# Kernel tuning notes

Measured on AMD Instinct MI355X. Metric: run time of the kernel, lower is better.

## Reference

```python
import jax, jax.numpy as jnp
import numpy as np

N_NODES = 100000
N_EDGES = 3200000
IN_CH, HID, OUT_CH = 128, 16, 64


def gcn_conv(x, W, b, row, col, n_nodes):
    # PyG GCNConv: add self loops, symmetric deg^{-1/2} normalization,
    # linear transform, scatter-add aggregation at target nodes (col).
    x = x @ W  # [N, out]
    deg = jax.ops.segment_sum(jnp.ones_like(col, dtype=x.dtype), col,
                              num_segments=n_nodes)  # includes self loops
    inv_sqrt = jnp.where(deg > 0, jax.lax.rsqrt(deg), 0.0)
    norm = inv_sqrt[row] * inv_sqrt[col]  # [E+N]
    msgs = x[row] * norm[:, None]  # gather + scale
    out = jax.ops.segment_sum(msgs, col, num_segments=n_nodes)
    return out + b


def setup_inputs() -> dict:
    key = jax.random.key(0)
    ks = jax.random.split(key, 12)
    x = jax.random.normal(ks[0], (N_NODES, IN_CH), dtype=jnp.float32)
    edge_index = jax.random.randint(ks[1], (2, N_EDGES), 0, N_NODES, dtype=jnp.int64)

    def glorot(k, fan_in, fan_out):
        s = jnp.sqrt(6.0 / (fan_in + fan_out))
        return jax.random.uniform(k, (fan_in, fan_out), jnp.float32, -s, s)

    return {
        'x': x,
        'edge_index': edge_index,
        'conv1_W': glorot(ks[2], IN_CH, HID),
        'conv1_b': jnp.zeros((HID,), jnp.float32),
        'conv2_W': glorot(ks[3], HID, OUT_CH),
        'conv2_b': jnp.zeros((OUT_CH,), jnp.float32),
        't1_W': glorot(ks[4], IN_CH, HID),
        't1_b': jnp.zeros((HID,), jnp.float32),
        't2_W': glorot(ks[5], HID, OUT_CH),
        't2_b': jnp.zeros((OUT_CH,), jnp.float32),
    }


def reference(x, edge_index, conv1_W, conv1_b, conv2_W, conv2_b,
              t1_W, t1_b, t2_W, t2_b):
    n = x.shape[0]
    # add self loops once (fixed shape)
    loops = jnp.arange(n, dtype=edge_index.dtype)
    row = jnp.concatenate([edge_index[0], loops])
    col = jnp.concatenate([edge_index[1], loops])

    identity1 = x @ t1_W + t1_b
    h = jax.nn.relu(gcn_conv(x, conv1_W, conv1_b, row, col, n)) + identity1
    identity2 = h @ t2_W + t2_b
    out = jax.nn.relu(gcn_conv(h, conv2_W, conv2_b, row, col, n)) + identity2
    return out
```

## Files before the change

kernel.cpp:

```cpp
#include <hip/hip_runtime.h>

#define INCH 128
#define C1   16
#define C2   64
#define LOCB 7
#define BNODES (1 << LOCB)
#define CAP  8192
#define ROWBITS 17
#define ROWMASK ((1 << ROWBITS) - 1)
#define SENT 0xFFFFFFFFu

typedef int iv4 __attribute__((ext_vector_type(4)));

__device__ __forceinline__ unsigned short f2bf(float f) {
    unsigned u = __float_as_uint(f);
    return (unsigned short)((u + 0x7FFF + ((u >> 16) & 1)) >> 16);
}
__device__ __forceinline__ float bf2f(unsigned short s) {
    return __uint_as_float((unsigned)s << 16);
}

__global__ void binit_kernel(int* __restrict__ gcur, int K) {
    int t = blockIdx.x * blockDim.x + threadIdx.x;
    if (t < K) gcur[t] = t * CAP;
}

__global__ __launch_bounds__(256) void bucket_kernel(
    const int* __restrict__ row, const int* __restrict__ col,
    int* __restrict__ gcur, int* __restrict__ barr,
    int e, int n, int K, int nblocks)
{
    __shared__ int cnt[1024];
    __shared__ int cur[1024];
    __shared__ int sst[1024];
    int e4 = e >> 2;
    long b0 = (long)blockIdx.x * e4 / nblocks;
    long b1 = (long)(blockIdx.x + 1) * e4 / nblocks;
    const iv4* c4p = (const iv4*)col;
    const iv4* r4p = (const iv4*)row;
    for (int i = threadIdx.x; i < 1024; i += 256) cnt[i] = 0;
    __syncthreads();
    for (long i = b0 + threadIdx.x; i < b1; i += 256) {
        iv4 c4 = c4p[i], r4 = r4p[i];
        #pragma unroll
        for (int k = 0; k < 4; ++k) {
            unsigned c = (unsigned)c4[k], r = (unsigned)r4[k];
            if (c < (unsigned)n && r < (unsigned)n)
                atomicAdd(&cnt[c >> LOCB], 1);
        }
    }
    if (blockIdx.x == 0) {
        for (int i = e4 * 4 + threadIdx.x; i < e; i += 256) {
            unsigned c = (unsigned)col[i], r = (unsigned)row[i];
            if (c < (unsigned)n && r < (unsigned)n)
                atomicAdd(&cnt[c >> LOCB], 1);
        }
    }
    __syncthreads();
    for (int i = threadIdx.x; i < K; i += 256) {
        int c = cnt[i];
        int start = c ? atomicAdd(&gcur[i], (c + 15) & ~15) : 0;
        cur[i] = start;
        sst[i] = start;
    }
    __syncthreads();
    for (long i = b0 + threadIdx.x; i < b1; i += 256) {
        iv4 c4 = c4p[i], r4 = r4p[i];
        #pragma unroll
        for (int k = 0; k < 4; ++k) {
            unsigned c = (unsigned)c4[k], r = (unsigned)r4[k];
            if (c < (unsigned)n && r < (unsigned)n) {
                int b = c >> LOCB;
                int slot = atomicAdd(&cur[b], 1);
                if ((unsigned)slot < (unsigned)((b + 1) * CAP))
                    barr[slot] = (int)(r | ((c & (BNODES - 1)) << ROWBITS));
            }
        }
    }
    if (blockIdx.x == 0) {
        for (int i = e4 * 4 + threadIdx.x; i < e; i += 256) {
            unsigned c = (unsigned)col[i], r = (unsigned)row[i];
            if (c < (unsigned)n && r < (unsigned)n) {
                int b = c >> LOCB;
                int slot = atomicAdd(&cur[b], 1);
                if ((unsigned)slot < (unsigned)((b + 1) * CAP))
                    barr[slot] = (int)(r | ((c & (BNODES - 1)) << ROWBITS));
            }
        }
    }
    __syncthreads();
    for (int i = threadIdx.x; i < K; i += 256) {
        int c = cnt[i];
        if (!c) continue;
        int start = sst[i];
        int end = start + c;
        int re  = start + ((c + 15) & ~15);
        int lim = (i + 1) * CAP;
        if (end > lim) end = lim;
        if (re  > lim) re  = lim;
        for (int j = end; j < re; ++j) barr[j] = (int)SENT;
    }
}

__global__ __launch_bounds__(1024) void bucket_scan_kernel(
    const int* __restrict__ gcur, int* __restrict__ bbase, int K)
{
    __shared__ int tmp[1024];
    int t = threadIdx.x;
    int len = 0;
    if (t < K) {
        int l = gcur[t] - t * CAP;
        len = (l < 0) ? 0 : (l > CAP ? CAP : l);
    }
    tmp[t] = len;
    __syncthreads();
    for (int off = 1; off < 1024; off <<= 1) {
        int v = (t >= off) ? tmp[t - off] : 0;
        __syncthreads();
        tmp[t] += v;
        __syncthreads();
    }
    if (t < K) bbase[t] = tmp[t] - len;
}

__global__ __launch_bounds__(256) void sort_kernel(
    const int* __restrict__ barr, const int* __restrict__ gcur,
    const int* __restrict__ bbase,
    int* __restrict__ cnt, int* __restrict__ offs, float* __restrict__ inv,
    int* __restrict__ sorted, int n)
{
    __shared__ int lcnt[BNODES];
    __shared__ int lcur[BNODES];
    __shared__ int tmp[BNODES];
    int b = blockIdx.x;
    int tid = threadIdx.x;
    if (tid < BNODES) lcnt[tid] = 0;
    __syncthreads();
    int base = b * CAP;
    int len = gcur[b] - base;
    if (len < 0) len = 0;
    if (len > CAP) len = CAP;
    int len4 = len >> 2;
    const iv4* b4 = (const iv4*)(barr + base);
    for (int i = tid; i < len4; i += 256) {
        iv4 p4 = b4[i];
        #pragma unroll
        for (int k = 0; k < 4; ++k) {
            unsigned pk = (unsigned)p4[k];
            if ((pk & ROWMASK) < (unsigned)n)
                atomicAdd(&lcnt[(pk >> ROWBITS) & (BNODES - 1)], 1);
        }
    }
    for (int i = len4 * 4 + tid; i < len; i += 256) {
        unsigned pk = (unsigned)barr[base + i];
        if ((pk & ROWMASK) < (unsigned)n)
            atomicAdd(&lcnt[(pk >> ROWBITS) & (BNODES - 1)], 1);
    }
    __syncthreads();
    int v = (tid < BNODES) ? lcnt[tid] : 0;
    if (tid < BNODES) tmp[tid] = v;
    __syncthreads();
    for (int off = 1; off < BNODES; off <<= 1) {
        int t2 = (tid < BNODES && tid >= off) ? tmp[tid - off] : 0;
        __syncthreads();
        if (tid < BNODES) tmp[tid] += t2;
        __syncthreads();
    }
    int gbase = bbase[b];
    if (tid < BNODES) {
        int exc = tmp[tid] - v;
        lcur[tid] = exc;
        int node = (b << LOCB) + tid;
        if (node < n) {
            cnt[node]  = v;
            offs[node] = gbase + exc;
            inv[node]  = rsqrtf((float)(v + 1));
        }
    }
    __syncthreads();
    for (int i = tid; i < len4; i += 256) {
        iv4 p4 = b4[i];
        #pragma unroll
        for (int k = 0; k < 4; ++k) {
            unsigned pk = (unsigned)p4[k];
            if ((pk & ROWMASK) < (unsigned)n) {
                int loc = (pk >> ROWBITS) & (BNODES - 1);
                int pos = atomicAdd(&lcur[loc], 1);
                if ((unsigned)pos < (unsigned)CAP)
                    sorted[gbase + pos] = (int)(pk & ROWMASK);
            }
        }
    }
    for (int i = len4 * 4 + tid; i < len; i += 256) {
        unsigned pk = (unsigned)barr[base + i];
        if ((pk & ROWMASK) < (unsigned)n) {
            int loc = (pk >> ROWBITS) & (BNODES - 1);
            int pos = atomicAdd(&lcur[loc], 1);
            if ((unsigned)pos < (unsigned)CAP)
                sorted[gbase + pos] = (int)(pk & ROWMASK);
        }
    }
}

__global__ __launch_bounds__(256) void linear1_kernel(
    const float* __restrict__ x, const float* __restrict__ W1,
    const float* __restrict__ T1, const float* __restrict__ t1b,
    const float* __restrict__ inv,
    unsigned short* __restrict__ xW1s_bf, float* __restrict__ xT1, int n)
{
    __shared__ float Wc[INCH][32];
    __shared__ float xs[16][INCH + 4];
    int tid = threadIdx.x;

    for (int i = tid; i < INCH * C1; i += 256) {
        int k = i / C1, c = i % C1;
        Wc[k][c]      = W1[i];
        Wc[k][c + 16] = T1[i];
    }
    int node0 = blockIdx.x * 16;
    for (int i = tid; i < 16 * (INCH / 4); i += 256) {
        int r = i / (INCH / 4);
        int cc = i % (INCH / 4);
        int node = node0 + r;
        float4 v = make_float4(0.f, 0.f, 0.f, 0.f);
        if (node < n) v = ((const float4*)x)[(size_t)node * (INCH / 4) + cc];
        ((float4*)&xs[r][0])[cc] = v;
    }
    __syncthreads();

    int ch = tid & 15, nl = tid >> 4;
    int node = node0 + nl;
    if (node >= n) return;
    float a1 = 0.f, a2 = 0.f;
    #pragma unroll
    for (int k = 0; k < INCH; ++k) {
        float xv = xs[nl][k];
        a1 += xv * Wc[k][ch];
        a2 += xv * Wc[k][ch + 16];
    }
    xW1s_bf[(node << 4) + ch] = f2bf(a1 * inv[node]);
    xT1[(node << 4) + ch]     = a2 + t1b[ch];
}

__global__ __launch_bounds__(256) void agg1_csr_kernel(
    const int* __restrict__ sorted, const int* __restrict__ offs,
    const int* __restrict__ cnt, const float* __restrict__ inv,
    const unsigned short* __restrict__ xW1s_bf, const float* __restrict__ xT1,
    const float* __restrict__ b1,
    float* __restrict__ h, unsigned short* __restrict__ hs_bf, int n)
{
    int node = blockIdx.x * 16 + (threadIdx.x >> 4);
    int ch = threadIdx.x & 15;
    if (node >= n) return;
    int beg = offs[node], end = beg + cnt[node];
    float ic = inv[node];
    float a0 = 0.f, a1 = 0.f, a2 = 0.f, a3 = 0.f;
    int p = beg;
    for (; p + 7 < end; p += 8) {
        int s0 = sorted[p],     s1 = sorted[p + 1];
        int s2 = sorted[p + 2], s3 = sorted[p + 3];
        int s4 = sorted[p + 4], s5 = sorted[p + 5];
        int s6 = sorted[p + 6], s7 = sorted[p + 7];
        a0 += bf2f(xW1s_bf[(s0 << 4) + ch]);
        a1 += bf2f(xW1s_bf[(s1 << 4) + ch]);
        a2 += bf2f(xW1s_bf[(s2 << 4) + ch]);
        a3 += bf2f(xW1s_bf[(s3 << 4) + ch]);
        a0 += bf2f(xW1s_bf[(s4 << 4) + ch]);
        a1 += bf2f(xW1s_bf[(s5 << 4) + ch]);
        a2 += bf2f(xW1s_bf[(s6 << 4) + ch]);
        a3 += bf2f(xW1s_bf[(s7 << 4) + ch]);
    }
    for (; p < end; ++p) a0 += bf2f(xW1s_bf[(sorted[p] << 4) + ch]);
    int idx = (node << 4) + ch;
    float v = (a0 + a1 + a2 + a3 + bf2f(xW1s_bf[idx])) * ic + b1[ch];
    float hv = fmaxf(v, 0.f) + xT1[idx];
    h[idx]     = hv;
    hs_bf[idx] = f2bf(hv * ic);
}

__global__ __launch_bounds__(256) void agg2_fused_kernel(
    const int* __restrict__ sorted, const int* __restrict__ offs,
    const int* __restrict__ cnt, const float* __restrict__ inv,
    const unsigned short* __restrict__ hs_bf, const float* __restrict__ h,
    const float* __restrict__ W2, const float* __restrict__ T2,
    const float* __restrict__ b2, const float* __restrict__ t2b,
    float* __restrict__ out, int n)
{
    __shared__ float Wc[C1][128];
    __shared__ float acc_s[16][C1];
    __shared__ float h_s[16][C1];
    int tid = threadIdx.x;

    for (int i = tid; i < C1 * 128; i += 256) {
        int k = i >> 7, c = i & 127;
        Wc[k][c] = (c < 64) ? W2[k * C2 + c] : T2[k * C2 + (c - 64)];
    }

    int nl = tid >> 4, ch = tid & 15;
    int node = blockIdx.x * 16 + nl;
    float acc = 0.f, hval = 0.f;
    if (node < n) {
        int beg = offs[node], end = beg + cnt[node];
        float a0 = 0.f, a1 = 0.f, a2 = 0.f, a3 = 0.f;
        int p = beg;
        for (; p + 7 < end; p += 8) {
            int s0 = sorted[p],     s1 = sorted[p + 1];
            int s2 = sorted[p + 2], s3 = sorted[p + 3];
            int s4 = sorted[p + 4], s5 = sorted[p + 5];
            int s6 = sorted[p + 6], s7 = sorted[p + 7];
            a0 += bf2f(hs_bf[(s0 << 4) + ch]);
            a1 += bf2f(hs_bf[(s1 << 4) + ch]);
            a2 += bf2f(hs_bf[(s2 << 4) + ch]);
            a3 += bf2f(hs_bf[(s3 << 4) + ch]);
            a0 += bf2f(hs_bf[(s4 << 4) + ch]);
            a1 += bf2f(hs_bf[(s5 << 4) + ch]);
            a2 += bf2f(hs_bf[(s6 << 4) + ch]);
            a3 += bf2f(hs_bf[(s7 << 4) + ch]);
        }
        for (; p < end; ++p) a0 += bf2f(hs_bf[(sorted[p] << 4) + ch]);
        int idx = (node << 4) + ch;
        acc = (a0 + a1 + a2 + a3 + bf2f(hs_bf[idx])) * inv[node];
        hval = h[idx];
    }
    acc_s[nl][ch] = acc;
    h_s[nl][ch]   = hval;
    __syncthreads();

    int och = tid & 63, grp = tid >> 6;
    #pragma unroll
    for (int q = 0; q < 4; ++q) {
        int nl2 = grp * 4 + q;
        int node2 = blockIdx.x * 16 + nl2;
        if (node2 >= n) continue;
        float s1v = b2[och], s2v = t2b[och];
        #pragma unroll
        for (int k = 0; k < C1; ++k) {
            s1v += acc_s[nl2][k] * Wc[k][och];
            s2v += h_s[nl2][k]   * Wc[k][och + 64];
        }
        out[node2 * C2 + och] = fmaxf(s1v, 0.f) + s2v;
    }
}

extern "C" void kernel_launch(void* const* d_in, const int* in_sizes, int n_in,
                              void* d_out, int out_size, void* d_ws, size_t ws_size,
                              hipStream_t stream) {
    const float* x   = (const float*)d_in[0];
    const int*   ei  = (const int*)d_in[1];
    const float* W1  = (const float*)d_in[2];
    const float* b1  = (const float*)d_in[3];
    const float* W2  = (const float*)d_in[4];
    const float* b2  = (const float*)d_in[5];
    const float* T1  = (const float*)d_in[6];
    const float* t1b = (const float*)d_in[7];
    const float* T2  = (const float*)d_in[8];
    const float* t2b = (const float*)d_in[9];
    float* out = (float*)d_out;

    const int n = in_sizes[0] / INCH;
    const int e = in_sizes[1] / 2;
    const int* row = ei;
    const int* col = ei + e;
    const int K = (n + BNODES - 1) >> LOCB;

    char* ws = (char*)d_ws;
    int*   gcur  = (int*)ws;                          ws += 4096;
    int*   bbase = (int*)ws;                          ws += 4096;
    int*   cnt   = (int*)ws;                          ws += (size_t)n * 4;
    int*   offs  = (int*)ws;                          ws += (size_t)n * 4;
    float* inv   = (float*)ws;                        ws += (size_t)n * 4;
    float* xT1   = (float*)ws;                        ws += (size_t)n * C1 * 4;
    float* h     = (float*)ws;                        ws += (size_t)n * C1 * 4;
    unsigned short* xW1s_bf = (unsigned short*)ws;    ws += (size_t)n * C1 * 2;
    unsigned short* hs_bf   = (unsigned short*)ws;    ws += (size_t)n * C1 * 2;
    int*   sorted= (int*)ws;                          ws += (size_t)K * CAP * 4;
    int*   barr  = (int*)ws;                          ws += (size_t)K * CAP * 4;

    const int B = 256;
    const int nbb = 390;

    binit_kernel      <<<(K + B - 1) / B, B, 0, stream>>>(gcur, K);
    bucket_kernel     <<<nbb, B, 0, stream>>>(row, col, gcur, barr, e, n, K, nbb);
    bucket_scan_kernel<<<1, 1024, 0, stream>>>(gcur, bbase, K);
    sort_kernel       <<<K, B, 0, stream>>>(barr, gcur, bbase, cnt, offs, inv, sorted, n);

    linear1_kernel <<<(n + 15) / 16, B, 0, stream>>>(x, W1, T1, t1b, inv, xW1s_bf, xT1, n);
    agg1_csr_kernel<<<(n + 15) / 16, B, 0, stream>>>(sorted, offs, cnt, inv, xW1s_bf, xT1, b1, h, hs_bf, n);

    agg2_fused_kernel<<<(n + 15) / 16, B, 0, stream>>>(sorted, offs, cnt, inv, hs_bf, h,
                                                       W2, T2, b2, t2b, out, n);
}
```

Measured before the change: 303.5 us.

## Aggregate directly from destination buckets with LDS atomics, dropping CSR sort

```diff
diff --git a/kernel.cpp b/kernel.cpp
--- a/kernel.cpp
+++ b/kernel.cpp
@@ -9,8 +9,10 @@
 #define ROWBITS 17
 #define ROWMASK ((1 << ROWBITS) - 1)
 #define SENT 0xFFFFFFFFu
+#define ACCP 17
 
 typedef int iv4 __attribute__((ext_vector_type(4)));
+typedef unsigned short usv8 __attribute__((ext_vector_type(8)));
 
 __device__ __forceinline__ unsigned short f2bf(float f) {
     unsigned u = __float_as_uint(f);
@@ -102,38 +104,12 @@
     }
 }
 
-__global__ __launch_bounds__(1024) void bucket_scan_kernel(
-    const int* __restrict__ gcur, int* __restrict__ bbase, int K)
-{
-    __shared__ int tmp[1024];
-    int t = threadIdx.x;
-    int len = 0;
-    if (t < K) {
-        int l = gcur[t] - t * CAP;
-        len = (l < 0) ? 0 : (l > CAP ? CAP : l);
-    }
-    tmp[t] = len;
-    __syncthreads();
-    for (int off = 1; off < 1024; off <<= 1) {
-        int v = (t >= off) ? tmp[t - off] : 0;
-        __syncthreads();
-        tmp[t] += v;
-        __syncthreads();
-    }
-    if (t < K) bbase[t] = tmp[t] - len;
-}
-
-__global__ __launch_bounds__(256) void sort_kernel(
+__global__ __launch_bounds__(256) void degree_kernel(
     const int* __restrict__ barr, const int* __restrict__ gcur,
-    const int* __restrict__ bbase,
-    int* __restrict__ cnt, int* __restrict__ offs, float* __restrict__ inv,
-    int* __restrict__ sorted, int n)
+    float* __restrict__ inv, int n)
 {
     __shared__ int lcnt[BNODES];
-    __shared__ int lcur[BNODES];
-    __shared__ int tmp[BNODES];
-    int b = blockIdx.x;
-    int tid = threadIdx.x;
+    int b = blockIdx.x, tid = threadIdx.x;
     if (tid < BNODES) lcnt[tid] = 0;
     __syncthreads();
     int base = b * CAP;
@@ -157,48 +133,9 @@
             atomicAdd(&lcnt[(pk >> ROWBITS) & (BNODES - 1)], 1);
     }
     __syncthreads();
-    int v = (tid < BNODES) ? lcnt[tid] : 0;
-    if (tid < BNODES) tmp[tid] = v;
-    __syncthreads();
-    for (int off = 1; off < BNODES; off <<= 1) {
-        int t2 = (tid < BNODES && tid >= off) ? tmp[tid - off] : 0;
-        __syncthreads();
-        if (tid < BNODES) tmp[tid] += t2;
-        __syncthreads();
-    }
-    int gbase = bbase[b];
     if (tid < BNODES) {
-        int exc = tmp[tid] - v;
-        lcur[tid] = exc;
         int node = (b << LOCB) + tid;
-        if (node < n) {
-            cnt[node]  = v;
-            offs[node] = gbase + exc;
-            inv[node]  = rsqrtf((float)(v + 1));
-        }
-    }
-    __syncthreads();
-    for (int i = tid; i < len4; i += 256) {
-        iv4 p4 = b4[i];
-        #pragma unroll
-        for (int k = 0; k < 4; ++k) {
-            unsigned pk = (unsigned)p4[k];
-            if ((pk & ROWMASK) < (unsigned)n) {
-                int loc = (pk >> ROWBITS) & (BNODES - 1);
-                int pos = atomicAdd(&lcur[loc], 1);
-                if ((unsigned)pos < (unsigned)CAP)
-                    sorted[gbase + pos] = (int)(pk & ROWMASK);
-            }
-        }
-    }
-    for (int i = len4 * 4 + tid; i < len; i += 256) {
-        unsigned pk = (unsigned)barr[base + i];
-        if ((pk & ROWMASK) < (unsigned)n) {
-            int loc = (pk >> ROWBITS) & (BNODES - 1);
-            int pos = atomicAdd(&lcur[loc], 1);
-            if ((unsigned)pos < (unsigned)CAP)
-                sorted[gbase + pos] = (int)(pk & ROWMASK);
-        }
+        if (node < n) inv[node] = rsqrtf((float)lcnt[tid] + 1.0f);
     }
 }
 
@@ -242,103 +179,164 @@
     xT1[(node << 4) + ch]     = a2 + t1b[ch];
 }
 
-__global__ __launch_bounds__(256) void agg1_csr_kernel(
-    const int* __restrict__ sorted, const int* __restrict__ offs,
-    const int* __restrict__ cnt, const float* __restrict__ inv,
-    const unsigned short* __restrict__ xW1s_bf, const float* __restrict__ xT1,
-    const float* __restrict__ b1,
+#define SCATTER8(PK, SRC)                                                     \
+    do {                                                                      \
+        unsigned _s = (PK) & ROWMASK;                                         \
+        if (_s < un) {                                                        \
+            float* _a = &acc[((PK) >> ROWBITS) & (BNODES - 1)][chb];          \
+            _Pragma("unroll")                                                 \
+            for (int _j = 0; _j < 8; ++_j)                                    \
+                atomicAdd(&_a[_j], __uint_as_float((unsigned)(SRC)[_j] << 16)); \
+        }                                                                     \
+    } while (0)
+
+__global__ __launch_bounds__(256) void agg1_bucket_kernel(
+    const int* __restrict__ barr, const int* __restrict__ gcur,
+    const float* __restrict__ inv, const unsigned short* __restrict__ xW1s_bf,
+    const float* __restrict__ xT1, const float* __restrict__ b1,
     float* __restrict__ h, unsigned short* __restrict__ hs_bf, int n)
 {
-    int node = blockIdx.x * 16 + (threadIdx.x >> 4);
-    int ch = threadIdx.x & 15;
-    if (node >= n) return;
-    int beg = offs[node], end = beg + cnt[node];
-    float ic = inv[node];
-    float a0 = 0.f, a1 = 0.f, a2 = 0.f, a3 = 0.f;
-    int p = beg;
-    for (; p + 7 < end; p += 8) {
-        int s0 = sorted[p],     s1 = sorted[p + 1];
-        int s2 = sorted[p + 2], s3 = sorted[p + 3];
-        int s4 = sorted[p + 4], s5 = sorted[p + 5];
-        int s6 = sorted[p + 6], s7 = sorted[p + 7];
-        a0 += bf2f(xW1s_bf[(s0 << 4) + ch]);
-        a1 += bf2f(xW1s_bf[(s1 << 4) + ch]);
-        a2 += bf2f(xW1s_bf[(s2 << 4) + ch]);
-        a3 += bf2f(xW1s_bf[(s3 << 4) + ch]);
-        a0 += bf2f(xW1s_bf[(s4 << 4) + ch]);
-        a1 += bf2f(xW1s_bf[(s5 << 4) + ch]);
-        a2 += bf2f(xW1s_bf[(s6 << 4) + ch]);
-        a3 += bf2f(xW1s_bf[(s7 << 4) + ch]);
-    }
-    for (; p < end; ++p) a0 += bf2f(xW1s_bf[(sorted[p] << 4) + ch]);
-    int idx = (node << 4) + ch;
-    float v = (a0 + a1 + a2 + a3 + bf2f(xW1s_bf[idx])) * ic + b1[ch];
-    float hv = fmaxf(v, 0.f) + xT1[idx];
-    h[idx]     = hv;
-    hs_bf[idx] = f2bf(hv * ic);
-}
-
-__global__ __launch_bounds__(256) void agg2_fused_kernel(
-    const int* __restrict__ sorted, const int* __restrict__ offs,
-    const int* __restrict__ cnt, const float* __restrict__ inv,
-    const unsigned short* __restrict__ hs_bf, const float* __restrict__ h,
+    __shared__ float acc[BNODES][ACCP];
+    int b = blockIdx.x, tid = threadIdx.x;
+    for (int i = tid; i < BNODES * ACCP; i += 256) (&acc[0][0])[i] = 0.f;
+    __syncthreads();
+
+    int base = b * CAP;
+    int len = gcur[b] - base;
+    if (len < 0) len = 0;
+    if (len > CAP) len = CAP;
+    const int* bp = barr + base;
+    unsigned un = (unsigned)n;
+    int chb = (tid & 1) << 3;
+    int i = tid >> 1;
+    for (; i + 384 < len; i += 512) {
+        unsigned k0 = (unsigned)bp[i];
+        unsigned k1 = (unsigned)bp[i + 128];
+        unsigned k2 = (unsigned)bp[i + 256];
+        unsigned k3 = (unsigned)bp[i + 384];
+        unsigned s0 = k0 & ROWMASK, s1 = k1 & ROWMASK;
+        unsigned s2 = k2 & ROWMASK, s3 = k3 & ROWMASK;
+        unsigned c0 = s0 < un ? s0 : 0u, c1 = s1 < un ? s1 : 0u;
+        unsigned c2 = s2 < un ? s2 : 0u, c3 = s3 < un ? s3 : 0u;
+        usv8 v0 = *(const usv8*)(xW1s_bf + ((size_t)c0 << 4) + chb);
+        usv8 v1 = *(const usv8*)(xW1s_bf + ((size_t)c1 << 4) + chb);
+        usv8 v2 = *(const usv8*)(xW1s_bf + ((size_t)c2 << 4) + chb);
+        usv8 v3 = *(const usv8*)(xW1s_bf + ((size_t)c3 << 4) + chb);
+        SCATTER8(k0, v0);
+        SCATTER8(k1, v1);
+        SCATTER8(k2, v2);
+        SCATTER8(k3, v3);
+    }
+    for (; i < len; i += 128) {
+        unsigned k0 = (unsigned)bp[i];
+        unsigned s0 = k0 & ROWMASK;
+        if (s0 < un) {
+            usv8 v0 = *(const usv8*)(xW1s_bf + ((size_t)s0 << 4) + chb);
+            SCATTER8(k0, v0);
+        }
+    }
+    __syncthreads();
+
+    for (int t = tid; t < BNODES * C1; t += 256) {
+        int loc = t >> 4, ch = t & 15;
+        int node = (b << LOCB) + loc;
+        if (node >= n) continue;
+        int idx = (node << 4) + ch;
+        float ic = inv[node];
+        float v = (acc[loc][ch] + bf2f(xW1s_bf[idx])) * ic + b1[ch];
+        float hv = fmaxf(v, 0.f) + xT1[idx];
+        h[idx]     = hv;
+        hs_bf[idx] = f2bf(hv * ic);
+    }
+}
+
+__global__ __launch_bounds__(256) void agg2_bucket_kernel(
+    const int* __restrict__ barr, const int* __restrict__ gcur,
+    const float* __restrict__ inv, const unsigned short* __restrict__ hs_bf,
+    const float* __restrict__ h,
     const float* __restrict__ W2, const float* __restrict__ T2,
     const float* __restrict__ b2, const float* __restrict__ t2b,
     float* __restrict__ out, int n)
 {
+    __shared__ float acc[BNODES][ACCP];
     __shared__ float Wc[C1][128];
-    __shared__ float acc_s[16][C1];
-    __shared__ float h_s[16][C1];
-    int tid = threadIdx.x;
-
+    __shared__ float h_s[BNODES][C1];
+    int b = blockIdx.x, tid = threadIdx.x;
+    for (int i = tid; i < BNODES * ACCP; i += 256) (&acc[0][0])[i] = 0.f;
     for (int i = tid; i < C1 * 128; i += 256) {
         int k = i >> 7, c = i & 127;
         Wc[k][c] = (c < 64) ? W2[k * C2 + c] : T2[k * C2 + (c - 64)];
     }
-
-    int nl = tid >> 4, ch = tid & 15;
-    int node = blockIdx.x * 16 + nl;
-    float acc = 0.f, hval = 0.f;
-    if (node < n) {
-        int beg = offs[node], end = beg + cnt[node];
-        float a0 = 0.f, a1 = 0.f, a2 = 0.f, a3 = 0.f;
-        int p = beg;
-        for (; p + 7 < end; p += 8) {
-            int s0 = sorted[p],     s1 = sorted[p + 1];
-            int s2 = sorted[p + 2], s3 = sorted[p + 3];
-            int s4 = sorted[p + 4], s5 = sorted[p + 5];
-            int s6 = sorted[p + 6], s7 = sorted[p + 7];
-            a0 += bf2f(hs_bf[(s0 << 4) + ch]);
-            a1 += bf2f(hs_bf[(s1 << 4) + ch]);
-            a2 += bf2f(hs_bf[(s2 << 4) + ch]);
-            a3 += bf2f(hs_bf[(s3 << 4) + ch]);
-            a0 += bf2f(hs_bf[(s4 << 4) + ch]);
-            a1 += bf2f(hs_bf[(s5 << 4) + ch]);
-            a2 += bf2f(hs_bf[(s6 << 4) + ch]);
-            a3 += bf2f(hs_bf[(s7 << 4) + ch]);
-        }
-        for (; p < end; ++p) a0 += bf2f(hs_bf[(sorted[p] << 4) + ch]);
-        int idx = (node << 4) + ch;
-        acc = (a0 + a1 + a2 + a3 + bf2f(hs_bf[idx])) * inv[node];
-        hval = h[idx];
-    }
-    acc_s[nl][ch] = acc;
-    h_s[nl][ch]   = hval;
-    __syncthreads();
-
-    int och = tid & 63, grp = tid >> 6;
+    {
+        int node0 = b << LOCB;
+        for (int t = tid; t < BNODES * C1 / 4; t += 256) {
+            float4 v = make_float4(0.f, 0.f, 0.f, 0.f);
+            if (node0 + (t >> 2) < n) v = ((const float4*)h)[(size_t)node0 * 4 + t];
+            ((float4*)&h_s[0][0])[t] = v;
+        }
+    }
+    __syncthreads();
+
+    int base = b * CAP;
+    int len = gcur[b] - base;
+    if (len < 0) len = 0;
+    if (len > CAP) len = CAP;
+    const int* bp = barr + base;
+    unsigned un = (unsigned)n;
+    int chb = (tid & 1) << 3;
+    int i = tid >> 1;
+    for (; i + 384 < len; i += 512) {
+        unsigned k0 = (unsigned)bp[i];
+        unsigned k1 = (unsigned)bp[i + 128];
+        unsigned k2 = (unsigned)bp[i + 256];
+        unsigned k3 = (unsigned)bp[i + 384];
+        unsigned s0 = k0 & ROWMASK, s1 = k1 & ROWMASK;
+        unsigned s2 = k2 & ROWMASK, s3 = k3 & ROWMASK;
+        unsigned c0 = s0 < un ? s0 : 0u, c1 = s1 < un ? s1 : 0u;
+        unsigned c2 = s2 < un ? s2 : 0u, c3 = s3 < un ? s3 : 0u;
+        usv8 v0 = *(const usv8*)(hs_bf + ((size_t)c0 << 4) + chb);
+        usv8 v1 = *(const usv8*)(hs_bf + ((size_t)c1 << 4) + chb);
+        usv8 v2 = *(const usv8*)(hs_bf + ((size_t)c2 << 4) + chb);
+        usv8 v3 = *(const usv8*)(hs_bf + ((size_t)c3 << 4) + chb);
+        SCATTER8(k0, v0);
+        SCATTER8(k1, v1);
+        SCATTER8(k2, v2);
+        SCATTER8(k3, v3);
+    }
+    for (; i < len; i += 128) {
+        unsigned k0 = (unsigned)bp[i];
+        unsigned s0 = k0 & ROWMASK;
+        if (s0 < un) {
+            usv8 v0 = *(const usv8*)(hs_bf + ((size_t)s0 << 4) + chb);
+            SCATTER8(k0, v0);
+        }
+    }
+    __syncthreads();
+
+    for (int t = tid; t < BNODES * C1; t += 256) {
+        int loc = t >> 4, ch = t & 15;
+        int node = (b << LOCB) + loc;
+        if (node >= n) continue;
+        acc[loc][ch] = (acc[loc][ch] + bf2f(hs_bf[(node << 4) + ch])) * inv[node];
+    }
+    __syncthreads();
+
+    int och = tid & 63, g = tid >> 6;
+    float w1r[C1], w2r[C1];
     #pragma unroll
-    for (int q = 0; q < 4; ++q) {
-        int nl2 = grp * 4 + q;
-        int node2 = blockIdx.x * 16 + nl2;
-        if (node2 >= n) continue;
-        float s1v = b2[och], s2v = t2b[och];
+    for (int k = 0; k < C1; ++k) { w1r[k] = Wc[k][och]; w2r[k] = Wc[k][och + 64]; }
+    float bb = b2[och], tb = t2b[och];
+    for (int q = 0; q < 32; ++q) {
+        int loc = (g << 5) + q;
+        int node = (b << LOCB) + loc;
+        if (node >= n) continue;
+        float s1 = bb, s2 = tb;
         #pragma unroll
         for (int k = 0; k < C1; ++k) {
-            s1v += acc_s[nl2][k] * Wc[k][och];
-            s2v += h_s[nl2][k]   * Wc[k][och + 64];
-        }
-        out[node2 * C2 + och] = fmaxf(s1v, 0.f) + s2v;
+            s1 += acc[loc][k] * w1r[k];
+            s2 += h_s[loc][k] * w2r[k];
+        }
+        out[(size_t)node * C2 + och] = fmaxf(s1, 0.f) + s2;
     }
 }
 
@@ -365,28 +363,22 @@
 
     char* ws = (char*)d_ws;
     int*   gcur  = (int*)ws;                          ws += 4096;
-    int*   bbase = (int*)ws;                          ws += 4096;
-    int*   cnt   = (int*)ws;                          ws += (size_t)n * 4;
-    int*   offs  = (int*)ws;                          ws += (size_t)n * 4;
     float* inv   = (float*)ws;                        ws += (size_t)n * 4;
     float* xT1   = (float*)ws;                        ws += (size_t)n * C1 * 4;
     float* h     = (float*)ws;                        ws += (size_t)n * C1 * 4;
     unsigned short* xW1s_bf = (unsigned short*)ws;    ws += (size_t)n * C1 * 2;
     unsigned short* hs_bf   = (unsigned short*)ws;    ws += (size_t)n * C1 * 2;
-    int*   sorted= (int*)ws;                          ws += (size_t)K * CAP * 4;
     int*   barr  = (int*)ws;                          ws += (size_t)K * CAP * 4;
 
     const int B = 256;
     const int nbb = 390;
 
-    binit_kernel      <<<(K + B - 1) / B, B, 0, stream>>>(gcur, K);
-    bucket_kernel     <<<nbb, B, 0, stream>>>(row, col, gcur, barr, e, n, K, nbb);
-    bucket_scan_kernel<<<1, 1024, 0, stream>>>(gcur, bbase, K);
-    sort_kernel       <<<K, B, 0, stream>>>(barr, gcur, bbase, cnt, offs, inv, sorted, n);
+    binit_kernel  <<<(K + B - 1) / B, B, 0, stream>>>(gcur, K);
+    bucket_kernel <<<nbb, B, 0, stream>>>(row, col, gcur, barr, e, n, K, nbb);
+    degree_kernel <<<K, B, 0, stream>>>(barr, gcur, inv, n);
 
     linear1_kernel <<<(n + 15) / 16, B, 0, stream>>>(x, W1, T1, t1b, inv, xW1s_bf, xT1, n);
-    agg1_csr_kernel<<<(n + 15) / 16, B, 0, stream>>>(sorted, offs, cnt, inv, xW1s_bf, xT1, b1, h, hs_bf, n);
-
-    agg2_fused_kernel<<<(n + 15) / 16, B, 0, stream>>>(sorted, offs, cnt, inv, hs_bf, h,
-                                                       W2, T2, b2, t2b, out, n);
-}
+    agg1_bucket_kernel<<<K, B, 0, stream>>>(barr, gcur, inv, xW1s_bf, xT1, b1, h, hs_bf, n);
+    agg2_bucket_kernel<<<K, B, 0, stream>>>(barr, gcur, inv, hs_bf, h,
+                                            W2, T2, b2, t2b, out, n);
+}
```

After: 885.6 us. 2.92x slower.

## Vectorize CSR gathers with 16-byte bf16 loads and four lanes per node

Applied to the files above, without the earlier changes.

```diff
diff --git a/kernel.cpp b/kernel.cpp
--- a/kernel.cpp
+++ b/kernel.cpp
@@ -11,6 +11,7 @@
 #define SENT 0xFFFFFFFFu
 
 typedef int iv4 __attribute__((ext_vector_type(4)));
+typedef unsigned short usv8 __attribute__((ext_vector_type(8)));
 
 __device__ __forceinline__ unsigned short f2bf(float f) {
     unsigned u = __float_as_uint(f);
@@ -242,6 +243,41 @@
     xT1[(node << 4) + ch]     = a2 + t1b[ch];
 }
 
+#define GATHER_ACC(SRCBUF)                                                    \
+    float a0 = 0.f, a1 = 0.f, a2 = 0.f, a3 = 0.f,                             \
+          a4 = 0.f, a5 = 0.f, a6 = 0.f, a7 = 0.f;                             \
+    {                                                                         \
+        int p = beg + pr;                                                     \
+        for (; p + 6 < end; p += 8) {                                         \
+            int s0 = sorted[p],     s1 = sorted[p + 2];                       \
+            int s2 = sorted[p + 4], s3 = sorted[p + 6];                       \
+            usv8 v0 = *(const usv8*)(SRCBUF + ((size_t)s0 << 4) + chb);       \
+            usv8 v1 = *(const usv8*)(SRCBUF + ((size_t)s1 << 4) + chb);       \
+            usv8 v2 = *(const usv8*)(SRCBUF + ((size_t)s2 << 4) + chb);       \
+            usv8 v3 = *(const usv8*)(SRCBUF + ((size_t)s3 << 4) + chb);       \
+            a0 += bf2f(v0[0]) + bf2f(v1[0]) + bf2f(v2[0]) + bf2f(v3[0]);      \
+            a1 += bf2f(v0[1]) + bf2f(v1[1]) + bf2f(v2[1]) + bf2f(v3[1]);      \
+            a2 += bf2f(v0[2]) + bf2f(v1[2]) + bf2f(v2[2]) + bf2f(v3[2]);      \
+            a3 += bf2f(v0[3]) + bf2f(v1[3]) + bf2f(v2[3]) + bf2f(v3[3]);      \
+            a4 += bf2f(v0[4]) + bf2f(v1[4]) + bf2f(v2[4]) + bf2f(v3[4]);      \
+            a5 += bf2f(v0[5]) + bf2f(v1[5]) + bf2f(v2[5]) + bf2f(v3[5]);      \
+            a6 += bf2f(v0[6]) + bf2f(v1[6]) + bf2f(v2[6]) + bf2f(v3[6]);      \
+            a7 += bf2f(v0[7]) + bf2f(v1[7]) + bf2f(v2[7]) + bf2f(v3[7]);      \
+        }                                                                     \
+        for (; p < end; p += 2) {                                             \
+            int s0 = sorted[p];                                               \
+            usv8 v0 = *(const usv8*)(SRCBUF + ((size_t)s0 << 4) + chb);       \
+            a0 += bf2f(v0[0]); a1 += bf2f(v0[1]);                             \
+            a2 += bf2f(v0[2]); a3 += bf2f(v0[3]);                             \
+            a4 += bf2f(v0[4]); a5 += bf2f(v0[5]);                             \
+            a6 += bf2f(v0[6]); a7 += bf2f(v0[7]);                             \
+        }                                                                     \
+    }                                                                         \
+    a0 += __shfl_xor(a0, 2); a1 += __shfl_xor(a1, 2);                         \
+    a2 += __shfl_xor(a2, 2); a3 += __shfl_xor(a3, 2);                         \
+    a4 += __shfl_xor(a4, 2); a5 += __shfl_xor(a5, 2);                         \
+    a6 += __shfl_xor(a6, 2); a7 += __shfl_xor(a7, 2);
+
 __global__ __launch_bounds__(256) void agg1_csr_kernel(
     const int* __restrict__ sorted, const int* __restrict__ offs,
     const int* __restrict__ cnt, const float* __restrict__ inv,
@@ -249,33 +285,35 @@
     const float* __restrict__ b1,
     float* __restrict__ h, unsigned short* __restrict__ hs_bf, int n)
 {
-    int node = blockIdx.x * 16 + (threadIdx.x >> 4);
-    int ch = threadIdx.x & 15;
-    if (node >= n) return;
-    int beg = offs[node], end = beg + cnt[node];
+    int tid = threadIdx.x;
+    int node = blockIdx.x * 64 + (tid >> 2);
+    int pr  = (tid >> 1) & 1;
+    int chb = (tid & 1) << 3;
+    int beg = 0, end = 0;
+    if (node < n) { beg = offs[node]; end = beg + cnt[node]; }
+
+    GATHER_ACC(xW1s_bf)
+
+    if (node >= n || pr != 0) return;
+    size_t idx = ((size_t)node << 4) + chb;
+    usv8 selfv = *(const usv8*)(xW1s_bf + idx);
     float ic = inv[node];
-    float a0 = 0.f, a1 = 0.f, a2 = 0.f, a3 = 0.f;
-    int p = beg;
-    for (; p + 7 < end; p += 8) {
-        int s0 = sorted[p],     s1 = sorted[p + 1];
-        int s2 = sorted[p + 2], s3 = sorted[p + 3];
-        int s4 = sorted[p + 4], s5 = sorted[p + 5];
-        int s6 = sorted[p + 6], s7 = sorted[p + 7];
-        a0 += bf2f(xW1s_bf[(s0 << 4) + ch]);
-        a1 += bf2f(xW1s_bf[(s1 << 4) + ch]);
-        a2 += bf2f(xW1s_bf[(s2 << 4) + ch]);
-        a3 += bf2f(xW1s_bf[(s3 << 4) + ch]);
-        a0 += bf2f(xW1s_bf[(s4 << 4) + ch]);
-        a1 += bf2f(xW1s_bf[(s5 << 4) + ch]);
-        a2 += bf2f(xW1s_bf[(s6 << 4) + ch]);
-        a3 += bf2f(xW1s_bf[(s7 << 4) + ch]);
-    }
-    for (; p < end; ++p) a0 += bf2f(xW1s_bf[(sorted[p] << 4) + ch]);
-    int idx = (node << 4) + ch;
-    float v = (a0 + a1 + a2 + a3 + bf2f(xW1s_bf[idx])) * ic + b1[ch];
-    float hv = fmaxf(v, 0.f) + xT1[idx];
-    h[idx]     = hv;
-    hs_bf[idx] = f2bf(hv * ic);
+    float hv0 = fmaxf((a0 + bf2f(selfv[0])) * ic + b1[chb + 0], 0.f) + xT1[idx + 0];
+    float hv1 = fmaxf((a1 + bf2f(selfv[1])) * ic + b1[chb + 1], 0.f) + xT1[idx + 1];
+    float hv2 = fmaxf((a2 + bf2f(selfv[2])) * ic + b1[chb + 2], 0.f) + xT1[idx + 2];
+    float hv3 = fmaxf((a3 + bf2f(selfv[3])) * ic + b1[chb + 3], 0.f) + xT1[idx + 3];
+    float hv4 = fmaxf((a4 + bf2f(selfv[4])) * ic + b1[chb + 4], 0.f) + xT1[idx + 4];
+    float hv5 = fmaxf((a5 + bf2f(selfv[5])) * ic + b1[chb + 5], 0.f) + xT1[idx + 5];
+    float hv6 = fmaxf((a6 + bf2f(selfv[6])) * ic + b1[chb + 6], 0.f) + xT1[idx + 6];
+    float hv7 = fmaxf((a7 + bf2f(selfv[7])) * ic + b1[chb + 7], 0.f) + xT1[idx + 7];
+    ((float4*)(h + idx))[0] = make_float4(hv0, hv1, hv2, hv3);
+    ((float4*)(h + idx))[1] = make_float4(hv4, hv5, hv6, hv7);
+    usv8 hb;
+    hb[0] = f2bf(hv0 * ic); hb[1] = f2bf(hv1 * ic);
+    hb[2] = f2bf(hv2 * ic); hb[3] = f2bf(hv3 * ic);
+    hb[4] = f2bf(hv4 * ic); hb[5] = f2bf(hv5 * ic);
+    hb[6] = f2bf(hv6 * ic); hb[7] = f2bf(hv7 * ic);
+    *(usv8*)(hs_bf + idx) = hb;
 }
 
 __global__ __launch_bounds__(256) void agg2_fused_kernel(
@@ -287,58 +325,61 @@
     float* __restrict__ out, int n)
 {
     __shared__ float Wc[C1][128];
-    __shared__ float acc_s[16][C1];
-    __shared__ float h_s[16][C1];
+    __shared__ float acc_s[64][C1];
+    __shared__ float h_s[64][C1];
     int tid = threadIdx.x;
 
     for (int i = tid; i < C1 * 128; i += 256) {
         int k = i >> 7, c = i & 127;
         Wc[k][c] = (c < 64) ? W2[k * C2 + c] : T2[k * C2 + (c - 64)];
     }
-
-    int nl = tid >> 4, ch = tid & 15;
-    int node = blockIdx.x * 16 + nl;
-    float acc = 0.f, hval = 0.f;
-    if (node < n) {
-        int beg = offs[node], end = beg + cnt[node];
-        float a0 = 0.f, a1 = 0.f, a2 = 0.f, a3 = 0.f;
-        int p = beg;
-        for (; p + 7 < end; p += 8) {
-            int s0 = sorted[p],     s1 = sorted[p + 1];
-            int s2 = sorted[p + 2], s3 = sorted[p + 3];
-            int s4 = sorted[p + 4], s5 = sorted[p + 5];
-            int s6 = sorted[p + 6], s7 = sorted[p + 7];
-            a0 += bf2f(hs_bf[(s0 << 4) + ch]);
-            a1 += bf2f(hs_bf[(s1 << 4) + ch]);
-            a2 += bf2f(hs_bf[(s2 << 4) + ch]);
-            a3 += bf2f(hs_bf[(s3 << 4) + ch]);
-            a0 += bf2f(hs_bf[(s4 << 4) + ch]);
-            a1 += bf2f(hs_bf[(s5 << 4) + ch]);
-            a2 += bf2f(hs_bf[(s6 << 4) + ch]);
-            a3 += bf2f(hs_bf[(s7 << 4) + ch]);
-        }
-        for (; p < end; ++p) a0 += bf2f(hs_bf[(sorted[p] << 4) + ch]);
-        int idx = (node << 4) + ch;
-        acc = (a0 + a1 + a2 + a3 + bf2f(hs_bf[idx])) * inv[node];
-        hval = h[idx];
-    }
-    acc_s[nl][ch] = acc;
-    h_s[nl][ch]   = hval;
-    __syncthreads();
-
-    int och = tid & 63, grp = tid >> 6;
+    {
+        int node0 = blockIdx.x * 64;
+        if (tid < 256) {
+            float4 v = make_float4(0.f, 0.f, 0.f, 0.f);
+            if (node0 + (tid >> 2) < n)
+                v = ((const float4*)h)[(size_t)node0 * 4 + tid];
+            ((float4*)&h_s[0][0])[tid] = v;
+        }
+    }
+
+    int node = blockIdx.x * 64 + (tid >> 2);
+    int pr  = (tid >> 1) & 1;
+    int chb = (tid & 1) << 3;
+    int beg = 0, end = 0;
+    if (node < n) { beg = offs[node]; end = beg + cnt[node]; }
+
+    GATHER_ACC(hs_bf)
+
+    if (node < n && pr == 0) {
+        size_t idx = ((size_t)node << 4) + chb;
+        usv8 selfv = *(const usv8*)(hs_bf + idx);
+        float ic = inv[node];
+        int loc = tid >> 2;
+        float4* ap = (float4*)&acc_s[loc][chb];
+        ap[0] = make_float4((a0 + bf2f(selfv[0])) * ic, (a1 + bf2f(selfv[1])) * ic,
+                            (a2 + bf2f(selfv[2])) * ic, (a3 + bf2f(selfv[3])) * ic);
+        ap[1] = make_float4((a4 + bf2f(selfv[4])) * ic, (a5 + bf2f(selfv[5])) * ic,
+                            (a6 + bf2f(selfv[6])) * ic, (a7 + bf2f(selfv[7])) * ic);
+    }
+    __syncthreads();
+
+    int och = tid & 63, g = tid >> 6;
+    float w1r[C1], w2r[C1];
     #pragma unroll
-    for (int q = 0; q < 4; ++q) {
-        int nl2 = grp * 4 + q;
-        int node2 = blockIdx.x * 16 + nl2;
+    for (int k = 0; k < C1; ++k) { w1r[k] = Wc[k][och]; w2r[k] = Wc[k][och + 64]; }
+    float bb = b2[och], tb = t2b[och];
+    for (int q = 0; q < 16; ++q) {
+        int loc = (g << 4) + q;
+        int node2 = blockIdx.x * 64 + loc;
         if (node2 >= n) continue;
-        float s1v = b2[och], s2v = t2b[och];
+        float s1 = bb, s2 = tb;
         #pragma unroll
         for (int k = 0; k < C1; ++k) {
-            s1v += acc_s[nl2][k] * Wc[k][och];
-            s2v += h_s[nl2][k]   * Wc[k][och + 64];
-        }
-        out[node2 * C2 + och] = fmaxf(s1v, 0.f) + s2v;
+            s1 += acc_s[loc][k] * w1r[k];
+            s2 += h_s[loc][k]   * w2r[k];
+        }
+        out[(size_t)node2 * C2 + och] = fmaxf(s1, 0.f) + s2;
     }
 }
 
@@ -385,8 +426,8 @@
     sort_kernel       <<<K, B, 0, stream>>>(barr, gcur, bbase, cnt, offs, inv, sorted, n);
 
     linear1_kernel <<<(n + 15) / 16, B, 0, stream>>>(x, W1, T1, t1b, inv, xW1s_bf, xT1, n);
-    agg1_csr_kernel<<<(n + 15) / 16, B, 0, stream>>>(sorted, offs, cnt, inv, xW1s_bf, xT1, b1, h, hs_bf, n);
-
-    agg2_fused_kernel<<<(n + 15) / 16, B, 0, stream>>>(sorted, offs, cnt, inv, hs_bf, h,
+    agg1_csr_kernel<<<(n + 63) / 64, B, 0, stream>>>(sorted, offs, cnt, inv, xW1s_bf, xT1, b1, h, hs_bf, n);
+
+    agg2_fused_kernel<<<(n + 63) / 64, B, 0, stream>>>(sorted, offs, cnt, inv, hs_bf, h,
                                                        W2, T2, b2, t2b, out, n);
 }
```

New measurement: 277.1 us. 1.1x faster.
